# Optimization experiments

Hardware: AMD Instinct MI355X
Metric: run time of the kernel (lower is better)

The kernel has to match this reference:

```python
import jax, jax.numpy as jnp
import numpy as np

G = 16          # spline grid_size
NT = 32         # num_tiles
NS = 2          # num_states
SD = 8          # state_dim
MAXLEN = 2048.0 # max_seq_len
SPREAD = 2.0    # position_spread
LN_EPS = 1e-5


def cubic_bspline(t):
    t = jnp.abs(t)
    r1 = 2.0 / 3.0 - t * t + 0.5 * t ** 3
    r2 = (1.0 / 6.0) * (2.0 - t) ** 3
    return jnp.where(t < 1.0, r1, jnp.where(t < 2.0, r2, jnp.zeros_like(t)))


def ternary(x):
    return jnp.where(x > 0.3, 1.0, jnp.where(x < -0.3, -1.0, 0.0)).astype(x.dtype)


def setup_inputs() -> dict:
    key = jax.random.key(0)
    ks = jax.random.split(key, 14)
    B, T, D = 4, 2048, 1024
    H = D // 4
    x = jax.random.normal(ks[0], (B, T, D), jnp.float32)
    positions = jnp.broadcast_to(jnp.arange(T, dtype=jnp.float32), (B, T))
    states = jax.random.randint(ks[1], (B, T), 0, NS)
    ln_gamma = jnp.ones((D,), jnp.float32)
    ln_beta = jnp.zeros((D,), jnp.float32)
    W1 = jax.random.normal(ks[2], (D, H), jnp.float32) * (1.0 / np.sqrt(D))
    b1 = jnp.zeros((H,), jnp.float32)
    W2 = jax.random.normal(ks[3], (H, 2), jnp.float32) * (1.0 / np.sqrt(H))
    b2 = jnp.zeros((2,), jnp.float32)
    spline_coeffs = jax.random.normal(ks[4], (NT, G, G, 3), jnp.float32) * 0.5
    spline_scales = jnp.ones((NT,), jnp.float32)
    directions = jax.random.normal(ks[5], (NT, D), jnp.float32) * 0.02
    state_signatures = jax.random.normal(ks[6], (NT, SD), jnp.float32) * 0.1
    state_emb = jax.random.normal(ks[7], (NS, SD), jnp.float32)
    state_mod = jnp.ones((NS, NT), jnp.float32)
    output_scale = jnp.ones((1,), jnp.float32) * 0.1
    return dict(x=x, positions=positions, states=states, ln_gamma=ln_gamma,
                ln_beta=ln_beta, W1=W1, b1=b1, W2=W2, b2=b2,
                spline_coeffs=spline_coeffs, spline_scales=spline_scales,
                directions=directions, state_signatures=state_signatures,
                state_emb=state_emb, state_mod=state_mod, output_scale=output_scale)


def reference(x, positions, states, ln_gamma, ln_beta, W1, b1, W2, b2,
              spline_coeffs, spline_scales, directions, state_signatures,
              state_emb, state_mod, output_scale):
    B, T, D = x.shape
    xf = x.reshape(-1, D)                               # [N, D]
    mu = jnp.mean(xf, axis=-1, keepdims=True)
    var = jnp.mean((xf - mu) ** 2, axis=-1, keepdims=True)
    xn = (xf - mu) / jnp.sqrt(var + LN_EPS) * ln_gamma + ln_beta

    # --- three-way routing ---
    sigs = jnp.sign(directions)                         # ternary signatures [NT, D]
    content = xn @ sigs.T                               # [N, NT]
    pos = positions.reshape(-1)
    pn = pos / MAXLEN * NT
    centers = jnp.arange(NT, dtype=xn.dtype)
    spatial = cubic_bspline((pn[:, None] - centers[None, :]) / SPREAD)  # [N, NT]
    st = states.reshape(-1)
    sv = state_emb[st]                                  # [N, SD]
    temporal = jax.nn.sigmoid(sv @ state_signatures.T)  # [N, NT]
    combined = content * spatial * temporal
    probs = jax.nn.softmax(combined * 5.0, axis=-1)
    tile_idx = jnp.argmax(combined, axis=-1)            # [N]
    tile_weights = jnp.take_along_axis(probs, tile_idx[:, None], axis=1)[:, 0]

    # --- compress to 2D spline coordinates ---
    h = jax.nn.gelu(xn @ W1 + b1, approximate=False)
    comp = jnp.tanh(h @ W2 + b2)                        # [N, 2]
    a, b = comp[:, 0], comp[:, 1]

    # --- ternary 2D spline per winning tile (vectorized dispatch) ---
    idx_a = jnp.clip(((a + 1.0) / 2.0 * G).astype(jnp.int32), 0, G - 1)
    idx_b = jnp.clip(((b + 1.0) / 2.0 * G).astype(jnp.int32), 0, G - 1)
    q = spline_coeffs + jax.lax.stop_gradient(ternary(spline_coeffs) - spline_coeffs)
    cell = q[tile_idx, idx_a, idx_b]                    # [N, 3]
    cs = 2.0 / G
    la = (a + 1.0 - idx_a.astype(a.dtype) * cs) / cs
    lb = (b + 1.0 - idx_b.astype(b.dtype) * cs) / cs
    scale = (cell[:, 0] + cell[:, 1] * la + cell[:, 2] * lb) * spline_scales[tile_idx]
    smod = state_mod[st, tile_idx]
    contrib = (scale * smod)[:, None] * directions[tile_idx]  # [N, D]

    out = x + contrib.reshape(B, T, D) * output_scale   # residual, eval (no dropout)
    return out
```

## Files before the change

### kernel.cpp

```cpp
#include <hip/hip_runtime.h>
#include <math.h>

#define NROWS 8192
#define DD    1024
#define HH    256
#define NTT   32
#define NCOLS 288
#define BM    32
#define BK    64
#define NW    12
#define HPS   292

typedef __attribute__((ext_vector_type(8))) __bf16 bf16x8;
typedef __attribute__((ext_vector_type(4))) float f32x4;
typedef __attribute__((ext_vector_type(8))) unsigned short ushort8_t;

static __device__ __forceinline__ unsigned short f2bf(float f) {
    unsigned int u = __float_as_uint(f);
    unsigned int r = (u + 0x7fffu + ((u >> 16) & 1u)) >> 16;
    return (unsigned short)r;
}

static __device__ __forceinline__ float sgnf(float x) {
    return x > 0.0f ? 1.0f : (x < 0.0f ? -1.0f : 0.0f);
}

static __device__ __forceinline__ float ternf(float x) {
    return x > 0.3f ? 1.0f : (x < -0.3f ? -1.0f : 0.0f);
}

static __device__ __forceinline__ float bspline(float u) {
    float t = fabsf(u);
    if (t < 1.0f) return 0.66666666666666663f - t * t + 0.5f * t * t * t;
    if (t < 2.0f) { float w = 2.0f - t; return 0.16666666666666666f * w * w * w; }
    return 0.0f;
}

__global__ __launch_bounds__(256) void k_prep_sig(const float* __restrict__ dirs,
                                                  const float* __restrict__ gamma,
                                                  const float* __restrict__ beta,
                                                  unsigned short* __restrict__ WT,
                                                  float* __restrict__ colsum,
                                                  float* __restrict__ bwv) {
    int r = blockIdx.x;
    int tid = threadIdx.x;
    if (tid < 8) {
        colsum[r * 8 + tid] = 0.0f;
        bwv[r * 8 + tid]    = 0.0f;
    }
    float4 v  = ((const float4*)(dirs + (size_t)r * DD))[tid];
    float4 g  = ((const float4*)gamma)[tid];
    float4 be = ((const float4*)beta)[tid];
    float s0 = sgnf(v.x), s1 = sgnf(v.y), s2 = sgnf(v.z), s3 = sgnf(v.w);
    ushort4 o;
    o.x = f2bf(s0 * g.x); o.y = f2bf(s1 * g.y);
    o.z = f2bf(s2 * g.z); o.w = f2bf(s3 * g.w);
    ((ushort4*)(WT + (size_t)(HH + r) * DD))[tid] = o;
    float ps = s0 * g.x + s1 * g.y + s2 * g.z + s3 * g.w;
    float pb = s0 * be.x + s1 * be.y + s2 * be.z + s3 * be.w;
#pragma unroll
    for (int off = 32; off; off >>= 1) {
        ps += __shfl_xor(ps, off);
        pb += __shfl_xor(pb, off);
    }
    __shared__ float red[8];
    int wid = tid >> 6, lane = tid & 63;
    if (lane == 0) { red[wid] = ps; red[wid + 4] = pb; }
    __syncthreads();
    if (tid == 0) {
        colsum[HH + r] = red[0] + red[1] + red[2] + red[3];
        bwv[HH + r]    = red[4] + red[5] + red[6] + red[7];
    }
}

__global__ __launch_bounds__(256) void k_prep_w1t(const float* __restrict__ W1,
                                                  const float* __restrict__ gamma,
                                                  const float* __restrict__ beta,
                                                  unsigned short* __restrict__ WT,
                                                  float* __restrict__ colsum,
                                                  float* __restrict__ bwv) {
    __shared__ float tile[32][33];
    __shared__ float redg[8][32];
    __shared__ float redb[8][32];
    int ktile = blockIdx.x;
    int ntile = blockIdx.y;
    int tx = threadIdx.x & 31;
    int ty = threadIdx.x >> 5;
    float sg = 0.f, sb = 0.f;
#pragma unroll
    for (int i = 0; i < 4; ++i) {
        int k = ktile * 32 + ty + i * 8;
        int n = ntile * 32 + tx;
        float w = W1[(size_t)k * HH + n];
        float gk = gamma[k];
        tile[ty + i * 8][tx] = w * gk;
        sg += w * gk;
        sb += w * beta[k];
    }
    redg[ty][tx] = sg;
    redb[ty][tx] = sb;
    __syncthreads();
#pragma unroll
    for (int i = 0; i < 4; ++i) {
        int n = ntile * 32 + ty + i * 8;
        int k = ktile * 32 + tx;
        WT[(size_t)n * DD + k] = f2bf(tile[tx][ty + i * 8]);
    }
    if (ty == 0) {
        float a = 0.f, c = 0.f;
#pragma unroll
        for (int k = 0; k < 8; ++k) { a += redg[k][tx]; c += redb[k][tx]; }
        int j = ntile * 32 + tx;
        atomicAdd(&colsum[j], a);
        atomicAdd(&bwv[j], c);
    }
}

__global__ __launch_bounds__(768) void k_fused(
    const float* __restrict__ x, const unsigned short* __restrict__ WT,
    const float* __restrict__ colsum, const float* __restrict__ bwv,
    const float* __restrict__ positions, const int* __restrict__ states,
    const float* __restrict__ b1, const float* __restrict__ W2,
    const float* __restrict__ b2, const float* __restrict__ spc,
    const float* __restrict__ sps, const float* __restrict__ dirs,
    const float* __restrict__ ssig, const float* __restrict__ semb,
    const float* __restrict__ smod, const float* __restrict__ oscale,
    float* __restrict__ out) {
    __shared__ short Al[2][BM * BK];
    __shared__ short Bl[2][NCOLS * BK];
    __shared__ float stats[BM][2];
    float* HPl = (float*)&Bl[0][0];

    int tid  = threadIdx.x;
    int row0 = blockIdx.x * BM;
    int lane = tid & 63;
    int wid  = tid >> 6;
    int wn = wid % 6, wm = wid / 6;
    int l15 = lane & 15, l4 = lane >> 4;

    int rA = tid >> 3;
    int g8 = tid & 7;
    const float* xrow = x + (size_t)(row0 + rA) * DD + g8 * 8;
    int aoff = (rA * 128 + g8 * 16) ^ ((rA & 7) << 4);

    float s = 0.f, sq = 0.f;
    float4 va, vb;
    f32x4 acc[3];
#pragma unroll
    for (int nf = 0; nf < 3; ++nf) acc[nf] = (f32x4){0.f, 0.f, 0.f, 0.f};

#define STAGE_B(kt, buf)                                                         \
    {                                                                            \
        _Pragma("unroll")                                                        \
        for (int ci = 0; ci < 3; ++ci) {                                         \
            int li = ci * 768 + tid;                                             \
            int r  = li >> 3;                                                    \
            int g  = li & 7;                                                     \
            const unsigned short* src =                                          \
                WT + (size_t)r * DD + (kt) * 64 + ((g * 8) ^ ((r & 7) << 3));    \
            __builtin_amdgcn_global_load_lds(                                    \
                (const __attribute__((address_space(1))) void*)(const void*)src, \
                (__attribute__((address_space(3))) void*)(void*)(Bl[buf] + li * 8), \
                16, 0, 0);                                                       \
        }                                                                        \
    }

#define LOAD_A(kt)                                                \
    if (wid < 4) {                                                \
        va = ((const float4*)(xrow + (kt) * 64))[0];              \
        vb = ((const float4*)(xrow + (kt) * 64))[1];              \
    }

#define WRITE_A(buf)                                                        \
    if (wid < 4) {                                                          \
        s  += (va.x + va.y + va.z + va.w) + (vb.x + vb.y + vb.z + vb.w);    \
        sq += (va.x*va.x + va.y*va.y + va.z*va.z + va.w*va.w)               \
            + (vb.x*vb.x + vb.y*vb.y + vb.z*vb.z + vb.w*vb.w);              \
        ushort8_t w;                                                        \
        w[0] = f2bf(va.x); w[1] = f2bf(va.y); w[2] = f2bf(va.z); w[3] = f2bf(va.w); \
        w[4] = f2bf(vb.x); w[5] = f2bf(vb.y); w[6] = f2bf(vb.z); w[7] = f2bf(vb.w); \
        *(ushort8_t*)((char*)Al[buf] + aoff) = w;                           \
    }

    STAGE_B(0, 0);
    LOAD_A(0);
    WRITE_A(0);
    __syncthreads();

    for (int kt = 0; kt < 16; ++kt) {
        int cur = kt & 1, nxt = cur ^ 1;
        if (kt < 15) {
            STAGE_B(kt + 1, nxt);
            LOAD_A(kt + 1);
        }
#pragma unroll
        for (int ks = 0; ks < 2; ++ks) {
            int ra = wm * 16 + l15;
            int ca = (ks * 64 + l4 * 16) ^ ((ra & 7) << 4);
            bf16x8 av = *(const bf16x8*)((const char*)Al[cur] + ra * 128 + ca);
            bf16x8 bv[3];
#pragma unroll
            for (int nf = 0; nf < 3; ++nf) {
                int rb = wn * 48 + nf * 16 + l15;
                int cb = (ks * 64 + l4 * 16) ^ ((rb & 7) << 4);
                bv[nf] = *(const bf16x8*)((const char*)Bl[cur] + rb * 128 + cb);
            }
#pragma unroll
            for (int nf = 0; nf < 3; ++nf)
                acc[nf] = __builtin_amdgcn_mfma_f32_16x16x32_bf16(av, bv[nf], acc[nf], 0, 0, 0);
        }
        if (kt < 15) WRITE_A(nxt);
        __syncthreads();
    }

    if (wid < 4) {
        s  += __shfl_xor(s, 1);  s  += __shfl_xor(s, 2);  s  += __shfl_xor(s, 4);
        sq += __shfl_xor(sq, 1); sq += __shfl_xor(sq, 2); sq += __shfl_xor(sq, 4);
        if (g8 == 0) {
            float mu  = s * (1.0f / DD);
            float var = sq * (1.0f / DD) - mu * mu;
            stats[rA][0] = mu;
            stats[rA][1] = rsqrtf(var + 1e-5f);
        }
    }
    __syncthreads();

#pragma unroll
    for (int nf = 0; nf < 3; ++nf) {
        int colg = wn * 48 + nf * 16 + l15;
        float cs = colsum[colg];
        float bw = bwv[colg];
        int r0 = wm * 16 + l4 * 4;
#pragma unroll
        for (int i = 0; i < 4; ++i) {
            float mu = stats[r0 + i][0], rs = stats[r0 + i][1];
            HPl[(r0 + i) * HPS + colg] = rs * acc[nf][i] - mu * rs * cs + bw;
        }
    }
    __syncthreads();

    float4 b1v = ((const float4*)b1)[lane];
    float w2a[4], w2b[4];
#pragma unroll
    for (int i = 0; i < 4; ++i) {
        int j = lane * 4 + i;
        w2a[i] = W2[2 * j];
        w2b[i] = W2[2 * j + 1];
    }
    float tvs[2] = {0.f, 0.f};
    if (lane < NTT) {
#pragma unroll
        for (int s2 = 0; s2 < 2; ++s2) {
            float d0 = 0.f;
#pragma unroll
            for (int k = 0; k < 8; ++k) d0 += semb[s2 * 8 + k] * ssig[lane * 8 + k];
            tvs[s2] = 1.0f / (1.0f + expf(-d0));
        }
    }
    float osc = oscale[0];
    float bb0 = b2[0], bb1 = b2[1];

    for (int r = wid; r < BM; r += NW) {
        int row = row0 + r;
        float4 hv = *(const float4*)&HPl[r * HPS + lane * 4];
        float hs[4] = {hv.x, hv.y, hv.z, hv.w};
        float bs[4] = {b1v.x, b1v.y, b1v.z, b1v.w};
        float sa = 0.f, sb2 = 0.f;
#pragma unroll
        for (int i = 0; i < 4; ++i) {
            float h = hs[i] + bs[i];
            float g = 0.5f * h * (1.0f + erff(h * 0.70710678118654752f));
            sa  += g * w2a[i];
            sb2 += g * w2b[i];
        }
#pragma unroll
        for (int off = 32; off; off >>= 1) {
            sa  += __shfl_xor(sa, off);
            sb2 += __shfl_xor(sb2, off);
        }
        float av2 = tanhf(sa + bb0);
        float bv2 = tanhf(sb2 + bb1);

        int st = states[row];
        float comb;
        if (lane < NTT) {
            float content = HPl[r * HPS + HH + lane];
            float pn = positions[row] * ((float)NTT / 2048.0f);
            float spv = bspline((pn - (float)lane) * 0.5f);
            comb = content * spv * tvs[st];
        } else {
            comb = -__builtin_inff();
        }
        int bi = lane;
#pragma unroll
        for (int off = 32; off; off >>= 1) {
            float ov = __shfl_xor(comb, off);
            int   oi = __shfl_xor(bi, off);
            if (ov > comb || (ov == comb && oi < bi)) { comb = ov; bi = oi; }
        }
        int ia = (int)((av2 + 1.0f) * 8.0f); ia = ia < 0 ? 0 : (ia > 15 ? 15 : ia);
        int ib = (int)((bv2 + 1.0f) * 8.0f); ib = ib < 0 ? 0 : (ib > 15 ? 15 : ib);
        const float* cc = spc + (((size_t)bi * 16 + ia) * 16 + ib) * 3;
        float c0 = ternf(cc[0]), c1 = ternf(cc[1]), c2 = ternf(cc[2]);
        float la = (av2 + 1.0f - (float)ia * 0.125f) * 8.0f;
        float lb = (bv2 + 1.0f - (float)ib * 0.125f) * 8.0f;
        float scale = (c0 + c1 * la + c2 * lb) * sps[bi];
        float cr = scale * smod[st * NTT + bi] * osc;

        const float4* xr = (const float4*)(x + (size_t)row * DD);
        const float4* dr = (const float4*)(dirs + (size_t)bi * DD);
        float4* orow = (float4*)(out + (size_t)row * DD);
#pragma unroll
        for (int i = 0; i < 4; ++i) {
            int idx = i * 64 + lane;
            float4 xv = xr[idx];
            float4 dv = dr[idx];
            float4 o;
            o.x = fmaf(cr, dv.x, xv.x);
            o.y = fmaf(cr, dv.y, xv.y);
            o.z = fmaf(cr, dv.z, xv.z);
            o.w = fmaf(cr, dv.w, xv.w);
            orow[idx] = o;
        }
    }
#undef STAGE_B
#undef LOAD_A
#undef WRITE_A
}

extern "C" void kernel_launch(void* const* d_in, const int* in_sizes, int n_in,
                              void* d_out, int out_size, void* d_ws, size_t ws_size,
                              hipStream_t stream) {
    const float* x     = (const float*)d_in[0];
    const float* pos   = (const float*)d_in[1];
    const int*   st    = (const int*)d_in[2];
    const float* gam   = (const float*)d_in[3];
    const float* bet   = (const float*)d_in[4];
    const float* W1    = (const float*)d_in[5];
    const float* b1    = (const float*)d_in[6];
    const float* W2    = (const float*)d_in[7];
    const float* b2    = (const float*)d_in[8];
    const float* spc   = (const float*)d_in[9];
    const float* sps   = (const float*)d_in[10];
    const float* dirs  = (const float*)d_in[11];
    const float* ssig  = (const float*)d_in[12];
    const float* semb  = (const float*)d_in[13];
    const float* smod  = (const float*)d_in[14];
    const float* oscal = (const float*)d_in[15];
    float* out = (float*)d_out;

    char* ws = (char*)d_ws;
    unsigned short* WT = (unsigned short*)ws;
    float* colsum = (float*)(ws + 589824);
    float* bwv    = (float*)(ws + 589824 + 1152);

    k_prep_sig<<<32, 256, 0, stream>>>(dirs, gam, bet, WT, colsum, bwv);
    k_prep_w1t<<<dim3(32, 8), 256, 0, stream>>>(W1, gam, bet, WT, colsum, bwv);
    k_fused<<<NROWS / BM, 768, 0, stream>>>(x, WT, colsum, bwv, pos, st, b1, W2, b2,
                                            spc, sps, dirs, ssig, semb, smod, oscal, out);
}
```

Before: 42.33 us.

## Prefetch x two K-steps ahead with manual waitcnts and merge prep kernels

The main GEMM loop is unrolled by two and double-buffers the x register loads, so activations for step kt+2 are fetched while step kt computes. __syncthreads is replaced by explicit s_waitcnt counts, raw s_barrier and sched_barrier fences to keep loads in flight across the barrier. The two weight-prep kernels are merged into one launch, with the accumulator zeroing moved to a hipMemsetAsync. A minimum of three blocks per SIMD is requested via launch_bounds, which could force register spills, and the hand-written waitcnt counts are fragile if the compiler reorders memory operations.

New measurement: 41.81 us. No clear change (-1.2%).

```diff
diff --git a/kernel.cpp b/kernel.cpp
--- a/kernel.cpp
+++ b/kernel.cpp
@@ -36,87 +36,80 @@
     return 0.0f;
 }
 
-__global__ __launch_bounds__(256) void k_prep_sig(const float* __restrict__ dirs,
-                                                  const float* __restrict__ gamma,
-                                                  const float* __restrict__ beta,
-                                                  unsigned short* __restrict__ WT,
-                                                  float* __restrict__ colsum,
-                                                  float* __restrict__ bwv) {
-    int r = blockIdx.x;
+__global__ __launch_bounds__(256) void k_prep(const float* __restrict__ W1,
+                                              const float* __restrict__ dirs,
+                                              const float* __restrict__ gamma,
+                                              const float* __restrict__ beta,
+                                              unsigned short* __restrict__ WT,
+                                              float* __restrict__ colsum,
+                                              float* __restrict__ bwv) {
+    int bid = blockIdx.x;
     int tid = threadIdx.x;
-    if (tid < 8) {
-        colsum[r * 8 + tid] = 0.0f;
-        bwv[r * 8 + tid]    = 0.0f;
-    }
-    float4 v  = ((const float4*)(dirs + (size_t)r * DD))[tid];
-    float4 g  = ((const float4*)gamma)[tid];
-    float4 be = ((const float4*)beta)[tid];
-    float s0 = sgnf(v.x), s1 = sgnf(v.y), s2 = sgnf(v.z), s3 = sgnf(v.w);
-    ushort4 o;
-    o.x = f2bf(s0 * g.x); o.y = f2bf(s1 * g.y);
-    o.z = f2bf(s2 * g.z); o.w = f2bf(s3 * g.w);
-    ((ushort4*)(WT + (size_t)(HH + r) * DD))[tid] = o;
-    float ps = s0 * g.x + s1 * g.y + s2 * g.z + s3 * g.w;
-    float pb = s0 * be.x + s1 * be.y + s2 * be.z + s3 * be.w;
-#pragma unroll
-    for (int off = 32; off; off >>= 1) {
-        ps += __shfl_xor(ps, off);
-        pb += __shfl_xor(pb, off);
-    }
-    __shared__ float red[8];
-    int wid = tid >> 6, lane = tid & 63;
-    if (lane == 0) { red[wid] = ps; red[wid + 4] = pb; }
-    __syncthreads();
-    if (tid == 0) {
-        colsum[HH + r] = red[0] + red[1] + red[2] + red[3];
-        bwv[HH + r]    = red[4] + red[5] + red[6] + red[7];
-    }
-}
-
-__global__ __launch_bounds__(256) void k_prep_w1t(const float* __restrict__ W1,
-                                                  const float* __restrict__ gamma,
-                                                  const float* __restrict__ beta,
-                                                  unsigned short* __restrict__ WT,
-                                                  float* __restrict__ colsum,
-                                                  float* __restrict__ bwv) {
-    __shared__ float tile[32][33];
-    __shared__ float redg[8][32];
-    __shared__ float redb[8][32];
-    int ktile = blockIdx.x;
-    int ntile = blockIdx.y;
-    int tx = threadIdx.x & 31;
-    int ty = threadIdx.x >> 5;
-    float sg = 0.f, sb = 0.f;
-#pragma unroll
-    for (int i = 0; i < 4; ++i) {
-        int k = ktile * 32 + ty + i * 8;
-        int n = ntile * 32 + tx;
-        float w = W1[(size_t)k * HH + n];
-        float gk = gamma[k];
-        tile[ty + i * 8][tx] = w * gk;
-        sg += w * gk;
-        sb += w * beta[k];
-    }
-    redg[ty][tx] = sg;
-    redb[ty][tx] = sb;
-    __syncthreads();
-#pragma unroll
-    for (int i = 0; i < 4; ++i) {
-        int n = ntile * 32 + ty + i * 8;
-        int k = ktile * 32 + tx;
-        WT[(size_t)n * DD + k] = f2bf(tile[tx][ty + i * 8]);
-    }
-    if (ty == 0) {
-        float a = 0.f, c = 0.f;
-#pragma unroll
-        for (int k = 0; k < 8; ++k) { a += redg[k][tx]; c += redb[k][tx]; }
-        int j = ntile * 32 + tx;
-        atomicAdd(&colsum[j], a);
-        atomicAdd(&bwv[j], c);
-    }
-}
-
-__global__ __launch_bounds__(768) void k_fused(
+    if (bid < 256) {
+        __shared__ float tile[32][33];
+        __shared__ float redg[8][32];
+        __shared__ float redb[8][32];
+        int ktile = bid & 31;
+        int ntile = bid >> 5;
+        int tx = tid & 31;
+        int ty = tid >> 5;
+        float sg = 0.f, sb = 0.f;
+#pragma unroll
+        for (int i = 0; i < 4; ++i) {
+            int k = ktile * 32 + ty + i * 8;
+            int n = ntile * 32 + tx;
+            float w = W1[(size_t)k * HH + n];
+            float gk = gamma[k];
+            tile[ty + i * 8][tx] = w * gk;
+            sg += w * gk;
+            sb += w * beta[k];
+        }
+        redg[ty][tx] = sg;
+        redb[ty][tx] = sb;
+        __syncthreads();
+#pragma unroll
+        for (int i = 0; i < 4; ++i) {
+            int n = ntile * 32 + ty + i * 8;
+            int k = ktile * 32 + tx;
+            WT[(size_t)n * DD + k] = f2bf(tile[tx][ty + i * 8]);
+        }
+        if (ty == 0) {
+            float a = 0.f, c = 0.f;
+#pragma unroll
+            for (int k = 0; k < 8; ++k) { a += redg[k][tx]; c += redb[k][tx]; }
+            int j = ntile * 32 + tx;
+            atomicAdd(&colsum[j], a);
+            atomicAdd(&bwv[j], c);
+        }
+    } else {
+        int r = bid - 256;
+        float4 v  = ((const float4*)(dirs + (size_t)r * DD))[tid];
+        float4 g  = ((const float4*)gamma)[tid];
+        float4 be = ((const float4*)beta)[tid];
+        float s0 = sgnf(v.x), s1 = sgnf(v.y), s2 = sgnf(v.z), s3 = sgnf(v.w);
+        ushort4 o;
+        o.x = f2bf(s0 * g.x); o.y = f2bf(s1 * g.y);
+        o.z = f2bf(s2 * g.z); o.w = f2bf(s3 * g.w);
+        ((ushort4*)(WT + (size_t)(HH + r) * DD))[tid] = o;
+        float ps = s0 * g.x + s1 * g.y + s2 * g.z + s3 * g.w;
+        float pb = s0 * be.x + s1 * be.y + s2 * be.z + s3 * be.w;
+#pragma unroll
+        for (int off = 32; off; off >>= 1) {
+            ps += __shfl_xor(ps, off);
+            pb += __shfl_xor(pb, off);
+        }
+        __shared__ float red[8];
+        int wid = tid >> 6, lane = tid & 63;
+        if (lane == 0) { red[wid] = ps; red[wid + 4] = pb; }
+        __syncthreads();
+        if (tid == 0) {
+            colsum[HH + r] = red[0] + red[1] + red[2] + red[3];
+            bwv[HH + r]    = red[4] + red[5] + red[6] + red[7];
+        }
+    }
+}
+
+__global__ __launch_bounds__(768, 3) void k_fused(
     const float* __restrict__ x, const unsigned short* __restrict__ WT,
     const float* __restrict__ colsum, const float* __restrict__ bwv,
     const float* __restrict__ positions, const int* __restrict__ states,
@@ -144,7 +137,7 @@
     int aoff = (rA * 128 + g8 * 16) ^ ((rA & 7) << 4);
 
     float s = 0.f, sq = 0.f;
-    float4 va, vb;
+    float4 x0a, x0b, x1a, x1b;
     f32x4 acc[3];
 #pragma unroll
     for (int nf = 0; nf < 3; ++nf) acc[nf] = (f32x4){0.f, 0.f, 0.f, 0.f};
@@ -165,53 +158,73 @@
         }                                                                        \
     }
 
-#define LOAD_A(kt)                                                \
-    if (wid < 4) {                                                \
-        va = ((const float4*)(xrow + (kt) * 64))[0];              \
-        vb = ((const float4*)(xrow + (kt) * 64))[1];              \
-    }
-
-#define WRITE_A(buf)                                                        \
-    if (wid < 4) {                                                          \
-        s  += (va.x + va.y + va.z + va.w) + (vb.x + vb.y + vb.z + vb.w);    \
-        sq += (va.x*va.x + va.y*va.y + va.z*va.z + va.w*va.w)               \
-            + (vb.x*vb.x + vb.y*vb.y + vb.z*vb.z + vb.w*vb.w);              \
-        ushort8_t w;                                                        \
-        w[0] = f2bf(va.x); w[1] = f2bf(va.y); w[2] = f2bf(va.z); w[3] = f2bf(va.w); \
-        w[4] = f2bf(vb.x); w[5] = f2bf(vb.y); w[6] = f2bf(vb.z); w[7] = f2bf(vb.w); \
-        *(ushort8_t*)((char*)Al[buf] + aoff) = w;                           \
-    }
-
+#define WRITE_A(XA, XB, buf)                                                    \
+    if (wid < 4) {                                                              \
+        s  += (XA.x + XA.y + XA.z + XA.w) + (XB.x + XB.y + XB.z + XB.w);        \
+        sq += (XA.x*XA.x + XA.y*XA.y + XA.z*XA.z + XA.w*XA.w)                   \
+            + (XB.x*XB.x + XB.y*XB.y + XB.z*XB.z + XB.w*XB.w);                  \
+        ushort8_t w;                                                            \
+        w[0] = f2bf(XA.x); w[1] = f2bf(XA.y); w[2] = f2bf(XA.z); w[3] = f2bf(XA.w); \
+        w[4] = f2bf(XB.x); w[5] = f2bf(XB.y); w[6] = f2bf(XB.z); w[7] = f2bf(XB.w); \
+        *(ushort8_t*)((char*)Al[buf] + aoff) = w;                               \
+    }
+
+#define COMPUTE(CUR)                                                            \
+    _Pragma("unroll")                                                           \
+    for (int ks = 0; ks < 2; ++ks) {                                            \
+        int ra = wm * 16 + l15;                                                 \
+        int ca = (ks * 64 + l4 * 16) ^ ((ra & 7) << 4);                         \
+        bf16x8 av = *(const bf16x8*)((const char*)Al[CUR] + ra * 128 + ca);     \
+        bf16x8 bv[3];                                                           \
+        _Pragma("unroll")                                                       \
+        for (int nf = 0; nf < 3; ++nf) {                                        \
+            int rb = wn * 48 + nf * 16 + l15;                                   \
+            int cb = (ks * 64 + l4 * 16) ^ ((rb & 7) << 4);                     \
+            bv[nf] = *(const bf16x8*)((const char*)Bl[CUR] + rb * 128 + cb);    \
+        }                                                                       \
+        _Pragma("unroll")                                                       \
+        for (int nf = 0; nf < 3; ++nf)                                          \
+            acc[nf] = __builtin_amdgcn_mfma_f32_16x16x32_bf16(av, bv[nf], acc[nf], 0, 0, 0); \
+    }
+
+#define STEP(kt, XCa, XCb, XIa, XIb, CUR, NXT)                                  \
+    {                                                                           \
+        if ((kt) <= 14) STAGE_B((kt) + 1, NXT);                                 \
+        __builtin_amdgcn_sched_barrier(0);                                      \
+        if ((kt) <= 13 && wid < 4) {                                            \
+            XIa = ((const float4*)(xrow + ((kt) + 2) * 64))[0];                 \
+            XIb = ((const float4*)(xrow + ((kt) + 2) * 64))[1];                 \
+        }                                                                       \
+        COMPUTE(CUR);                                                           \
+        if ((kt) <= 14) WRITE_A(XCa, XCb, NXT);                                 \
+        if ((kt) <= 13) {                                                       \
+            if (wid < 4) asm volatile("s_waitcnt vmcnt(2) lgkmcnt(0)" ::: "memory"); \
+            else         asm volatile("s_waitcnt vmcnt(0)" ::: "memory");       \
+        } else if ((kt) == 14) {                                                \
+            if (wid < 4) asm volatile("s_waitcnt vmcnt(0) lgkmcnt(0)" ::: "memory"); \
+            else         asm volatile("s_waitcnt vmcnt(0)" ::: "memory");       \
+        }                                                                       \
+        if ((kt) <= 14) {                                                       \
+            __builtin_amdgcn_s_barrier();                                       \
+            __builtin_amdgcn_sched_barrier(0);                                  \
+        }                                                                       \
+    }
+
+    if (wid < 4) {
+        x0a = ((const float4*)(xrow))[0];
+        x0b = ((const float4*)(xrow))[1];
+        x1a = ((const float4*)(xrow + 64))[0];
+        x1b = ((const float4*)(xrow + 64))[1];
+    }
     STAGE_B(0, 0);
-    LOAD_A(0);
-    WRITE_A(0);
+    WRITE_A(x0a, x0b, 0);
     __syncthreads();
 
-    for (int kt = 0; kt < 16; ++kt) {
-        int cur = kt & 1, nxt = cur ^ 1;
-        if (kt < 15) {
-            STAGE_B(kt + 1, nxt);
-            LOAD_A(kt + 1);
-        }
-#pragma unroll
-        for (int ks = 0; ks < 2; ++ks) {
-            int ra = wm * 16 + l15;
-            int ca = (ks * 64 + l4 * 16) ^ ((ra & 7) << 4);
-            bf16x8 av = *(const bf16x8*)((const char*)Al[cur] + ra * 128 + ca);
-            bf16x8 bv[3];
-#pragma unroll
-            for (int nf = 0; nf < 3; ++nf) {
-                int rb = wn * 48 + nf * 16 + l15;
-                int cb = (ks * 64 + l4 * 16) ^ ((rb & 7) << 4);
-                bv[nf] = *(const bf16x8*)((const char*)Bl[cur] + rb * 128 + cb);
-            }
-#pragma unroll
-            for (int nf = 0; nf < 3; ++nf)
-                acc[nf] = __builtin_amdgcn_mfma_f32_16x16x32_bf16(av, bv[nf], acc[nf], 0, 0, 0);
-        }
-        if (kt < 15) WRITE_A(nxt);
-        __syncthreads();
-    }
+    for (int kt = 0; kt < 16; kt += 2) {
+        STEP(kt,     x1a, x1b, x0a, x0b, 0, 1);
+        STEP(kt + 1, x0a, x0b, x1a, x1b, 1, 0);
+    }
+    __syncthreads();
 
     if (wid < 4) {
         s  += __shfl_xor(s, 1);  s  += __shfl_xor(s, 2);  s  += __shfl_xor(s, 4);
@@ -324,8 +337,9 @@
         }
     }
 #undef STAGE_B
-#undef LOAD_A
 #undef WRITE_A
+#undef COMPUTE
+#undef STEP
 }
 
 extern "C" void kernel_launch(void* const* d_in, const int* in_sizes, int n_in,
@@ -352,10 +366,10 @@
     char* ws = (char*)d_ws;
     unsigned short* WT = (unsigned short*)ws;
     float* colsum = (float*)(ws + 589824);
-    float* bwv    = (float*)(ws + 589824 + 1152);
-
-    k_prep_sig<<<32, 256, 0, stream>>>(dirs, gam, bet, WT, colsum, bwv);
-    k_prep_w1t<<<dim3(32, 8), 256, 0, stream>>>(W1, gam, bet, WT, colsum, bwv);
+    float* bwv    = (float*)(ws + 589824 + 288 * 4);
+
+    hipMemsetAsync(colsum, 0, 2 * 288 * sizeof(float), stream);
+    k_prep<<<288, 256, 0, stream>>>(W1, dirs, gam, bet, WT, colsum, bwv);
     k_fused<<<NROWS / BM, 768, 0, stream>>>(x, WT, colsum, bwv, pos, st, b1, W2, b2,
                                             spc, sps, dirs, ssig, semb, smod, oscal, out);
 }
```
